# Optimization experiments

Measured on AMD Instinct MI355X. Metric: run time of the kernel, lower is better.

## Reference

```python
import jax, jax.numpy as jnp
import numpy as np

N_NODES = 100000
N_EDGES = 1600000
N_GRAPHS = 64
D_IN, D_HID, D_LAT = 2, 64, 32


def setup_inputs() -> dict:
    key = jax.random.key(0)
    k1, k2, k3, k4, k5, k6, k7 = jax.random.split(key, 7)
    x = jax.random.normal(k1, (N_NODES, D_IN), dtype=jnp.float32)
    edge_index = jax.random.randint(k2, (2, N_EDGES), 0, N_NODES, dtype=jnp.int64)
    batch = jnp.sort(jax.random.randint(k3, (N_NODES,), 0, N_GRAPHS, dtype=jnp.int64))
    # GCNConv params (glorot-ish scale)
    W1 = jax.random.normal(k4, (D_IN, D_HID), dtype=jnp.float32) * (1.0 / np.sqrt(D_IN))
    b1 = jnp.zeros((D_HID,), dtype=jnp.float32)
    W2 = jax.random.normal(k5, (D_HID, D_LAT), dtype=jnp.float32) * (1.0 / np.sqrt(D_HID))
    b2 = jnp.zeros((D_LAT,), dtype=jnp.float32)
    return {"x": x, "W1": W1, "b1": b1, "W2": W2, "b2": b2,
            "edge_index": edge_index, "batch": batch}


def _gcn_conv(x, W, b, src, dst, n_nodes):
    """PyG GCNConv: add self-loops, symmetric deg^-1/2 normalization, linear, scatter-add."""
    h = x @ W  # [N, d_out]
    loop = jnp.arange(n_nodes, dtype=src.dtype)
    src_f = jnp.concatenate([src, loop])
    dst_f = jnp.concatenate([dst, loop])
    deg = jax.ops.segment_sum(jnp.ones_like(dst_f, dtype=h.dtype), dst_f,
                              num_segments=n_nodes)  # in-degree incl. self-loop
    dis = jnp.where(deg > 0, jax.lax.rsqrt(deg), 0.0)
    norm = dis[src_f] * dis[dst_f]  # [E+N]
    msg = h[src_f] * norm[:, None]  # edge gather (memory-bound)
    out = jax.ops.segment_sum(msg, dst_f, num_segments=n_nodes)
    return out + b


def reference(x, W1, b1, W2, b2, edge_index, batch):
    src, dst = edge_index[0], edge_index[1]
    n = x.shape[0]
    h = jax.nn.relu(_gcn_conv(x, W1, b1, src, dst, n))
    z = _gcn_conv(h, W2, b2, src, dst, n)
    # global_mean_pool over graph ids
    sums = jax.ops.segment_sum(z, batch, num_segments=N_GRAPHS)
    cnts = jax.ops.segment_sum(jnp.ones((n,), dtype=z.dtype), batch,
                               num_segments=N_GRAPHS)
    return sums / jnp.maximum(cnts, 1.0)[:, None]
```

## Files before the change

kernel.cpp:

```cpp
#include <hip/hip_runtime.h>
#include <hip/hip_fp16.h>

#define N_NODES  100000
#define N_EDGES  1600000
#define N_GRAPHS 64
#define NBUCK    391
#define NBLK     256
#define CHUNK    (N_EDGES / NBLK)

#define OFF_GSTART 0
#define OFF_ROWPTR 128
#define OFF_DIS    100224
#define OFF_S      200320
#define OFF_CSR    400384
#define OFF_Q      2000384
#define OFF_BHIST  2000384
#define OFF_BOFFL  2100736
#define OFF_BSUM   2201088
#define OFF_BSTART 2201600
#define OFF_TMP    2202112

__device__ __forceinline__ int excl_scan_256(int v, int* wsum) {
  int t = threadIdx.x, lane = t & 63, w = t >> 6;
  int x = v;
#pragma unroll
  for (int off = 1; off < 64; off <<= 1) {
    int y = __shfl_up(x, off, 64);
    if (lane >= off) x += y;
  }
  if (lane == 63) wsum[w] = x;
  __syncthreads();
  if (t == 0) {
    int r = 0;
#pragma unroll
    for (int i = 0; i < 4; ++i) { int tv = wsum[i]; wsum[i] = r; r += tv; }
  }
  __syncthreads();
  return x - v + wsum[w];
}

__device__ __forceinline__ int excl_scan_512(int v, int* wsum) {
  int t = threadIdx.x, lane = t & 63, w = t >> 6;
  int x = v;
#pragma unroll
  for (int off = 1; off < 64; off <<= 1) {
    int y = __shfl_up(x, off, 64);
    if (lane >= off) x += y;
  }
  if (lane == 63) wsum[w] = x;
  __syncthreads();
  if (t == 0) {
    int r = 0;
#pragma unroll
    for (int i = 0; i < 8; ++i) { int tv = wsum[i]; wsum[i] = r; r += tv; }
  }
  __syncthreads();
  return x - v + wsum[w];
}

__global__ void k_hist(const int* __restrict__ dst, int* __restrict__ bhist) {
  __shared__ int hist[NBUCK];
  int t = threadIdx.x, k = blockIdx.x;
  for (int b = t; b < NBUCK; b += 256) hist[b] = 0;
  __syncthreads();
  int e0 = k * CHUNK, e1 = e0 + CHUNK;
  for (int e = e0 + t; e < e1; e += 256) atomicAdd(&hist[dst[e] >> 8], 1);
  __syncthreads();
  for (int b = t; b < NBUCK; b += 256) bhist[b * NBLK + k] = hist[b];
}

__global__ void k_bounds(const int* __restrict__ batch, int* __restrict__ gstart) {
  int i = blockIdx.x * 256 + threadIdx.x;
  if (i >= N_NODES) return;
  int bi = batch[i];
  if (i == 0) {
    for (int g = 0; g <= bi; ++g) gstart[g] = 0;
  } else {
    int bp = batch[i - 1];
    for (int g = bp + 1; g <= bi; ++g) gstart[g] = i;
  }
  if (i == N_NODES - 1) {
    for (int g = bi + 1; g <= N_GRAPHS; ++g) gstart[g] = N_NODES;
  }
}

__global__ void k_scan_a(const int* __restrict__ bhist, int* __restrict__ boffl,
                         int* __restrict__ bsum) {
  __shared__ int wsum[4];
  int t = threadIdx.x, b = blockIdx.x;
  int v = bhist[b * NBLK + t];
  int ex = excl_scan_256(v, wsum);
  boffl[b * NBLK + t] = ex;
  if (t == NBLK - 1) bsum[b] = ex + v;
}

__global__ void k_scan_b(const int* __restrict__ bsum, int* __restrict__ bstart) {
  __shared__ int wsum[8];
  int t = threadIdx.x;
  int v = (t < NBUCK) ? bsum[t] : 0;
  int ex = excl_scan_512(v, wsum);
  if (t <= NBUCK) bstart[t] = ex;
}

__global__ void k_scatter(const int* __restrict__ src, const int* __restrict__ dst,
                          const int* __restrict__ bstart, const int* __restrict__ boffl,
                          int* __restrict__ tmp) {
  __shared__ int sbase[NBUCK];
  __shared__ int fill[NBUCK];
  int t = threadIdx.x, k = blockIdx.x;
  for (int b = t; b < NBUCK; b += 256) {
    sbase[b] = bstart[b] + boffl[b * NBLK + k];
    fill[b] = 0;
  }
  __syncthreads();
  int e0 = k * CHUNK, e1 = e0 + CHUNK;
  for (int e = e0 + t; e < e1; e += 256) {
    int s_ = src[e], d_ = dst[e];
    int b = d_ >> 8;
    int pos = sbase[b] + atomicAdd(&fill[b], 1);
    tmp[pos] = (s_ << 8) | (d_ & 255);
  }
}

__global__ void k_fine(const int* __restrict__ tmp, const int* __restrict__ bstart,
                       const float* __restrict__ x, int* __restrict__ csr_src,
                       int* __restrict__ row_ptr, float* __restrict__ dis,
                       float2* __restrict__ s) {
  __shared__ int hist[256];
  __shared__ int fill[256];
  __shared__ int wsum[4];
  int t = threadIdx.x, b = blockIdx.x;
  int base_n = b << 8;
  int e0 = bstart[b], e1 = bstart[b + 1];
  hist[t] = 0;
  __syncthreads();
  for (int e = e0 + t; e < e1; e += 256) atomicAdd(&hist[tmp[e] & 255], 1);
  __syncthreads();
  int h = hist[t];
  int ex = excl_scan_256(h, wsum);
  hist[t] = ex;
  fill[t] = 0;
  int nn = min(256, N_NODES - base_n);
  if (t < nn) {
    int v = base_n + t;
    row_ptr[v] = e0 + ex;
    float dv = rsqrtf((float)(h + 1));
    dis[v] = dv;
    float2 xv = ((const float2*)x)[v];
    s[v] = make_float2(xv.x * dv, xv.y * dv);
  }
  if (b == NBUCK - 1 && t == 0) row_ptr[N_NODES] = e1;
  __syncthreads();
  for (int e = e0 + t; e < e1; e += 256) {
    int p = tmp[e];
    int fine = p & 255;
    int pos = e0 + hist[fine] + atomicAdd(&fill[fine], 1);
    csr_src[pos] = p >> 8;
  }
}

__global__ void k_layer1(const float2* __restrict__ s, const float* __restrict__ dis,
                         const int* __restrict__ row_ptr, const int* __restrict__ csr_src,
                         const float* __restrict__ W1, const float* __restrict__ b1,
                         const float* __restrict__ W2, __half2* __restrict__ qh) {
  __shared__ float sW1[128];
  __shared__ float sb1[64];
  __shared__ float sW2[2048];
  int tid = threadIdx.x;
  for (int i = tid; i < 128; i += 256) sW1[i] = W1[i];
  for (int i = tid; i < 64; i += 256) sb1[i] = b1[i];
  for (int i = tid; i < 2048; i += 256) sW2[i] = W2[i];
  __syncthreads();
  int v = blockIdx.x * 256 + tid;
  if (v >= N_NODES) return;
  int beg = row_ptr[v], end = row_ptr[v + 1];
  float2 sv = s[v];
  float t0 = sv.x, t1 = sv.y;
  int k = beg;
  for (; k + 4 <= end; k += 4) {
    int u0 = csr_src[k], u1 = csr_src[k + 1], u2 = csr_src[k + 2], u3 = csr_src[k + 3];
    float2 a = s[u0], b = s[u1], c = s[u2], d = s[u3];
    t0 += a.x + b.x + c.x + d.x;
    t1 += a.y + b.y + c.y + d.y;
  }
  for (; k < end; ++k) {
    float2 su = s[csr_src[k]];
    t0 += su.x;
    t1 += su.y;
  }
  float dv = dis[v];
  t0 *= dv;
  t1 *= dv;
  float acc[32];
#pragma unroll
  for (int m = 0; m < 32; ++m) acc[m] = 0.f;
  for (int j = 0; j < 64; ++j) {
    float r = fmaxf(fmaf(t0, sW1[j], fmaf(t1, sW1[64 + j], sb1[j])), 0.f);
#pragma unroll
    for (int m = 0; m < 32; ++m) acc[m] = fmaf(r, sW2[j * 32 + m], acc[m]);
  }
  int buf[16];
#pragma unroll
  for (int m = 0; m < 16; ++m) {
    __half2 h = __floats2half2_rn(acc[2 * m] * dv, acc[2 * m + 1] * dv);
    buf[m] = *reinterpret_cast<int*>(&h);
  }
  int4* dst4 = (int4*)&qh[v * 16];
  dst4[0] = make_int4(buf[0], buf[1], buf[2], buf[3]);
  dst4[1] = make_int4(buf[4], buf[5], buf[6], buf[7]);
  dst4[2] = make_int4(buf[8], buf[9], buf[10], buf[11]);
  dst4[3] = make_int4(buf[12], buf[13], buf[14], buf[15]);
}

__global__ void k_layer2(const __half2* __restrict__ qh, const float* __restrict__ dis,
                         const int* __restrict__ row_ptr, const int* __restrict__ csr_src,
                         const int* __restrict__ batch, float* __restrict__ pooled) {
  __shared__ float2 red[16][16];
  int t = threadIdx.x;
  int f2 = t & 15;
  int rg = t >> 4;
  int vb = blockIdx.x * 64;
  int nlast = min(vb + 63, N_NODES - 1);
  bool uniform = (batch[vb] == batch[nlast]);
  int v0 = vb + rg * 4;
  int v1 = min(v0 + 4, N_NODES);
  float2 acc = make_float2(0.f, 0.f);
  int curg = (v0 < N_NODES) ? batch[v0] : -1;
  for (int v = v0; v < v1; ++v) {
    if (!uniform) {
      int g = batch[v];
      if (g != curg) {
        atomicAdd(&pooled[curg * 32 + 2 * f2], acc.x);
        atomicAdd(&pooled[curg * 32 + 2 * f2 + 1], acc.y);
        acc = make_float2(0.f, 0.f);
        curg = g;
      }
    }
    int e0 = row_ptr[v], e1 = row_ptr[v + 1];
    float2 z = __half22float2(qh[v * 16 + f2]);
    int k = e0;
    for (; k + 4 <= e1; k += 4) {
      int u0 = csr_src[k], u1 = csr_src[k + 1], u2 = csr_src[k + 2], u3 = csr_src[k + 3];
      __half2 a = qh[u0 * 16 + f2];
      __half2 b = qh[u1 * 16 + f2];
      __half2 c = qh[u2 * 16 + f2];
      __half2 d = qh[u3 * 16 + f2];
      float2 fa = __half22float2(a), fb = __half22float2(b);
      float2 fc = __half22float2(c), fd = __half22float2(d);
      z.x += (fa.x + fb.x) + (fc.x + fd.x);
      z.y += (fa.y + fb.y) + (fc.y + fd.y);
    }
    for (; k < e1; ++k) {
      float2 f = __half22float2(qh[csr_src[k] * 16 + f2]);
      z.x += f.x;
      z.y += f.y;
    }
    float dv = dis[v];
    acc.x = fmaf(z.x, dv, acc.x);
    acc.y = fmaf(z.y, dv, acc.y);
  }
  if (uniform) {
    red[rg][f2] = acc;
    __syncthreads();
    if (t < 16) {
      float2 ssum = make_float2(0.f, 0.f);
#pragma unroll
      for (int r = 0; r < 16; ++r) {
        ssum.x += red[r][t].x;
        ssum.y += red[r][t].y;
      }
      int g = batch[vb];
      atomicAdd(&pooled[g * 32 + 2 * t], ssum.x);
      atomicAdd(&pooled[g * 32 + 2 * t + 1], ssum.y);
    }
  } else if (curg >= 0) {
    atomicAdd(&pooled[curg * 32 + 2 * f2], acc.x);
    atomicAdd(&pooled[curg * 32 + 2 * f2 + 1], acc.y);
  }
}

__global__ void k_final(float* __restrict__ out, const int* __restrict__ gstart,
                        const float* __restrict__ b2) {
  int i = blockIdx.x * 256 + threadIdx.x;
  if (i < N_GRAPHS * 32) {
    int g = i >> 5, l = i & 31;
    int c = gstart[g + 1] - gstart[g];
    out[i] = (c > 0) ? out[i] / (float)c + b2[l] : 0.f;
  }
}

extern "C" void kernel_launch(void* const* d_in, const int* in_sizes, int n_in,
                              void* d_out, int out_size, void* d_ws, size_t ws_size,
                              hipStream_t stream) {
  (void)in_sizes; (void)n_in; (void)out_size; (void)ws_size;
  const float* x   = (const float*)d_in[0];
  const float* W1  = (const float*)d_in[1];
  const float* b1  = (const float*)d_in[2];
  const float* W2  = (const float*)d_in[3];
  const float* b2  = (const float*)d_in[4];
  const int* edge  = (const int*)d_in[5];
  const int* batch = (const int*)d_in[6];
  const int* src = edge;
  const int* dst = edge + N_EDGES;
  float* out = (float*)d_out;

  int* ws      = (int*)d_ws;
  int* gstart  = ws + OFF_GSTART;
  int* row_ptr = ws + OFF_ROWPTR;
  float* dis   = (float*)(ws + OFF_DIS);
  float2* s    = (float2*)(ws + OFF_S);
  int* csr_src = ws + OFF_CSR;
  __half2* qh  = (__half2*)(ws + OFF_Q);
  int* bhist   = ws + OFF_BHIST;
  int* boffl   = ws + OFF_BOFFL;
  int* bsum    = ws + OFF_BSUM;
  int* bstart  = ws + OFF_BSTART;
  int* tmp     = ws + OFF_TMP;

  hipMemsetAsync(out, 0, (size_t)(N_GRAPHS * 32) * sizeof(float), stream);

  k_hist<<<NBLK, 256, 0, stream>>>(dst, bhist);
  k_bounds<<<(N_NODES + 255) / 256, 256, 0, stream>>>(batch, gstart);
  k_scan_a<<<NBUCK, 256, 0, stream>>>(bhist, boffl, bsum);
  k_scan_b<<<1, 512, 0, stream>>>(bsum, bstart);
  k_scatter<<<NBLK, 256, 0, stream>>>(src, dst, bstart, boffl, tmp);
  k_fine<<<NBUCK, 256, 0, stream>>>(tmp, bstart, x, csr_src, row_ptr, dis, s);
  k_layer1<<<(N_NODES + 255) / 256, 256, 0, stream>>>(s, dis, row_ptr, csr_src,
                                                      W1, b1, W2, qh);
  k_layer2<<<(N_NODES + 63) / 64, 256, 0, stream>>>(qh, dis, row_ptr, csr_src,
                                                    batch, out);
  k_final<<<8, 256, 0, stream>>>(out, gstart, b2);
}
```

Baseline: 110.6 us.

## Split layer-2 features into lo/hi half tables and fold small launches into scans

The layer-1 output is written as two separate half-precision tables, one per 16-feature half. Layer-2 blocks each gather only one half, with blocks for the same node range interleaved across halves, so each gathered row is 32 bytes and each table's working set is smaller and more cache-friendly. The graph-bounds computation moves into the first scan kernel, and the output zeroing moves into the second scan kernel, which removes one launch and one memset. Layer 1 also loads its weights as float4 from shared memory, and layer 2 unrolls the edge gather by 8. The cost is twice as many layer-2 blocks, each re-reading row_ptr and csr_src, and extra atomics into the pooled output.

```diff
diff --git a/kernel.cpp b/kernel.cpp
--- a/kernel.cpp
+++ b/kernel.cpp
@@ -7,13 +7,15 @@
 #define NBUCK    391
 #define NBLK     256
 #define CHUNK    (N_EDGES / NBLK)
+#define NODEBLK  1563
 
 #define OFF_GSTART 0
 #define OFF_ROWPTR 128
 #define OFF_DIS    100224
 #define OFF_S      200320
 #define OFF_CSR    400384
-#define OFF_Q      2000384
+#define OFF_QLO    2000384
+#define OFF_QHI    2800512
 #define OFF_BHIST  2000384
 #define OFF_BOFFL  2100736
 #define OFF_BSUM   2201088
@@ -69,34 +71,35 @@
   for (int b = t; b < NBUCK; b += 256) bhist[b * NBLK + k] = hist[b];
 }
 
-__global__ void k_bounds(const int* __restrict__ batch, int* __restrict__ gstart) {
-  int i = blockIdx.x * 256 + threadIdx.x;
-  if (i >= N_NODES) return;
-  int bi = batch[i];
-  if (i == 0) {
-    for (int g = 0; g <= bi; ++g) gstart[g] = 0;
-  } else {
-    int bp = batch[i - 1];
-    for (int g = bp + 1; g <= bi; ++g) gstart[g] = i;
-  }
-  if (i == N_NODES - 1) {
-    for (int g = bi + 1; g <= N_GRAPHS; ++g) gstart[g] = N_NODES;
-  }
-}
-
 __global__ void k_scan_a(const int* __restrict__ bhist, int* __restrict__ boffl,
-                         int* __restrict__ bsum) {
+                         int* __restrict__ bsum, const int* __restrict__ batch,
+                         int* __restrict__ gstart) {
   __shared__ int wsum[4];
   int t = threadIdx.x, b = blockIdx.x;
+  int i = b * 256 + t;
+  if (i < N_NODES) {
+    int bi = batch[i];
+    if (i == 0) {
+      for (int g = 0; g <= bi; ++g) gstart[g] = 0;
+    } else {
+      int bp = batch[i - 1];
+      for (int g = bp + 1; g <= bi; ++g) gstart[g] = i;
+    }
+    if (i == N_NODES - 1) {
+      for (int g = bi + 1; g <= N_GRAPHS; ++g) gstart[g] = N_NODES;
+    }
+  }
   int v = bhist[b * NBLK + t];
   int ex = excl_scan_256(v, wsum);
   boffl[b * NBLK + t] = ex;
   if (t == NBLK - 1) bsum[b] = ex + v;
 }
 
-__global__ void k_scan_b(const int* __restrict__ bsum, int* __restrict__ bstart) {
+__global__ void k_scan_b(const int* __restrict__ bsum, int* __restrict__ bstart,
+                         float* __restrict__ pooled) {
   __shared__ int wsum[8];
   int t = threadIdx.x;
+  for (int i = t; i < N_GRAPHS * 32; i += 512) pooled[i] = 0.f;
   int v = (t < NBUCK) ? bsum[t] : 0;
   int ex = excl_scan_512(v, wsum);
   if (t <= NBUCK) bstart[t] = ex;
@@ -162,14 +165,13 @@
 __global__ void k_layer1(const float2* __restrict__ s, const float* __restrict__ dis,
                          const int* __restrict__ row_ptr, const int* __restrict__ csr_src,
                          const float* __restrict__ W1, const float* __restrict__ b1,
-                         const float* __restrict__ W2, __half2* __restrict__ qh) {
-  __shared__ float sW1[128];
-  __shared__ float sb1[64];
-  __shared__ float sW2[2048];
+                         const float* __restrict__ W2, int4* __restrict__ q_lo,
+                         int4* __restrict__ q_hi) {
+  __shared__ float4 sWB[64];
+  __shared__ float4 sW2[512];
   int tid = threadIdx.x;
-  for (int i = tid; i < 128; i += 256) sW1[i] = W1[i];
-  for (int i = tid; i < 64; i += 256) sb1[i] = b1[i];
-  for (int i = tid; i < 2048; i += 256) sW2[i] = W2[i];
+  if (tid < 64) sWB[tid] = make_float4(W1[tid], W1[64 + tid], b1[tid], 0.f);
+  for (int i = tid; i < 512; i += 256) sW2[i] = ((const float4*)W2)[i];
   __syncthreads();
   int v = blockIdx.x * 256 + tid;
   if (v >= N_NODES) return;
@@ -180,8 +182,8 @@
   for (; k + 4 <= end; k += 4) {
     int u0 = csr_src[k], u1 = csr_src[k + 1], u2 = csr_src[k + 2], u3 = csr_src[k + 3];
     float2 a = s[u0], b = s[u1], c = s[u2], d = s[u3];
-    t0 += a.x + b.x + c.x + d.x;
-    t1 += a.y + b.y + c.y + d.y;
+    t0 += (a.x + b.x) + (c.x + d.x);
+    t1 += (a.y + b.y) + (c.y + d.y);
   }
   for (; k < end; ++k) {
     float2 su = s[csr_src[k]];
@@ -191,67 +193,94 @@
   float dv = dis[v];
   t0 *= dv;
   t1 *= dv;
-  float acc[32];
-#pragma unroll
-  for (int m = 0; m < 32; ++m) acc[m] = 0.f;
+  float4 a4[8];
+#pragma unroll
+  for (int m = 0; m < 8; ++m) a4[m] = make_float4(0.f, 0.f, 0.f, 0.f);
   for (int j = 0; j < 64; ++j) {
-    float r = fmaxf(fmaf(t0, sW1[j], fmaf(t1, sW1[64 + j], sb1[j])), 0.f);
-#pragma unroll
-    for (int m = 0; m < 32; ++m) acc[m] = fmaf(r, sW2[j * 32 + m], acc[m]);
-  }
-  int buf[16];
-#pragma unroll
-  for (int m = 0; m < 16; ++m) {
-    __half2 h = __floats2half2_rn(acc[2 * m] * dv, acc[2 * m + 1] * dv);
-    buf[m] = *reinterpret_cast<int*>(&h);
-  }
-  int4* dst4 = (int4*)&qh[v * 16];
-  dst4[0] = make_int4(buf[0], buf[1], buf[2], buf[3]);
-  dst4[1] = make_int4(buf[4], buf[5], buf[6], buf[7]);
-  dst4[2] = make_int4(buf[8], buf[9], buf[10], buf[11]);
-  dst4[3] = make_int4(buf[12], buf[13], buf[14], buf[15]);
-}
-
-__global__ void k_layer2(const __half2* __restrict__ qh, const float* __restrict__ dis,
-                         const int* __restrict__ row_ptr, const int* __restrict__ csr_src,
-                         const int* __restrict__ batch, float* __restrict__ pooled) {
-  __shared__ float2 red[16][16];
+    float4 wb = sWB[j];
+    float r = fmaxf(fmaf(t0, wb.x, fmaf(t1, wb.y, wb.z)), 0.f);
+#pragma unroll
+    for (int m = 0; m < 8; ++m) {
+      float4 w = sW2[j * 8 + m];
+      a4[m].x = fmaf(r, w.x, a4[m].x);
+      a4[m].y = fmaf(r, w.y, a4[m].y);
+      a4[m].z = fmaf(r, w.z, a4[m].z);
+      a4[m].w = fmaf(r, w.w, a4[m].w);
+    }
+  }
+  int pk[16];
+#pragma unroll
+  for (int m = 0; m < 8; ++m) {
+    __half2 h0 = __floats2half2_rn(a4[m].x * dv, a4[m].y * dv);
+    __half2 h1 = __floats2half2_rn(a4[m].z * dv, a4[m].w * dv);
+    pk[2 * m]     = *reinterpret_cast<int*>(&h0);
+    pk[2 * m + 1] = *reinterpret_cast<int*>(&h1);
+  }
+  q_lo[v * 2]     = make_int4(pk[0], pk[1], pk[2], pk[3]);
+  q_lo[v * 2 + 1] = make_int4(pk[4], pk[5], pk[6], pk[7]);
+  q_hi[v * 2]     = make_int4(pk[8], pk[9], pk[10], pk[11]);
+  q_hi[v * 2 + 1] = make_int4(pk[12], pk[13], pk[14], pk[15]);
+}
+
+__global__ void k_layer2(const __half2* __restrict__ q_lo, const __half2* __restrict__ q_hi,
+                         const float* __restrict__ dis, const int* __restrict__ row_ptr,
+                         const int* __restrict__ csr_src, const int* __restrict__ batch,
+                         float* __restrict__ pooled) {
+  __shared__ float2 red[32][8];
+  int w = blockIdx.x;
+  int h = (w & 7) >> 2;
+  int sub = (w >> 3) * 4 + (w & 3);
+  if (sub >= NODEBLK) return;
+  const __half2* q = h ? q_hi : q_lo;
   int t = threadIdx.x;
-  int f2 = t & 15;
-  int rg = t >> 4;
-  int vb = blockIdx.x * 64;
+  int fp = t & 7;
+  int rg = t >> 3;
+  int vb = sub * 64;
   int nlast = min(vb + 63, N_NODES - 1);
   bool uniform = (batch[vb] == batch[nlast]);
-  int v0 = vb + rg * 4;
-  int v1 = min(v0 + 4, N_NODES);
+  int v0 = vb + rg * 2;
+  int v1 = min(v0 + 2, N_NODES);
   float2 acc = make_float2(0.f, 0.f);
   int curg = (v0 < N_NODES) ? batch[v0] : -1;
+  int obase = h * 16 + 2 * fp;
   for (int v = v0; v < v1; ++v) {
     if (!uniform) {
       int g = batch[v];
       if (g != curg) {
-        atomicAdd(&pooled[curg * 32 + 2 * f2], acc.x);
-        atomicAdd(&pooled[curg * 32 + 2 * f2 + 1], acc.y);
+        atomicAdd(&pooled[curg * 32 + obase], acc.x);
+        atomicAdd(&pooled[curg * 32 + obase + 1], acc.y);
         acc = make_float2(0.f, 0.f);
         curg = g;
       }
     }
     int e0 = row_ptr[v], e1 = row_ptr[v + 1];
-    float2 z = __half22float2(qh[v * 16 + f2]);
+    float2 z = __half22float2(q[v * 8 + fp]);
     int k = e0;
+    for (; k + 8 <= e1; k += 8) {
+      int u0 = csr_src[k],     u1 = csr_src[k + 1], u2 = csr_src[k + 2], u3 = csr_src[k + 3];
+      int u4 = csr_src[k + 4], u5 = csr_src[k + 5], u6 = csr_src[k + 6], u7 = csr_src[k + 7];
+      float2 f0 = __half22float2(q[u0 * 8 + fp]);
+      float2 f1 = __half22float2(q[u1 * 8 + fp]);
+      float2 f2 = __half22float2(q[u2 * 8 + fp]);
+      float2 f3 = __half22float2(q[u3 * 8 + fp]);
+      float2 f4 = __half22float2(q[u4 * 8 + fp]);
+      float2 f5 = __half22float2(q[u5 * 8 + fp]);
+      float2 f6 = __half22float2(q[u6 * 8 + fp]);
+      float2 f7 = __half22float2(q[u7 * 8 + fp]);
+      z.x += ((f0.x + f1.x) + (f2.x + f3.x)) + ((f4.x + f5.x) + (f6.x + f7.x));
+      z.y += ((f0.y + f1.y) + (f2.y + f3.y)) + ((f4.y + f5.y) + (f6.y + f7.y));
+    }
     for (; k + 4 <= e1; k += 4) {
       int u0 = csr_src[k], u1 = csr_src[k + 1], u2 = csr_src[k + 2], u3 = csr_src[k + 3];
-      __half2 a = qh[u0 * 16 + f2];
-      __half2 b = qh[u1 * 16 + f2];
-      __half2 c = qh[u2 * 16 + f2];
-      __half2 d = qh[u3 * 16 + f2];
-      float2 fa = __half22float2(a), fb = __half22float2(b);
-      float2 fc = __half22float2(c), fd = __half22float2(d);
-      z.x += (fa.x + fb.x) + (fc.x + fd.x);
-      z.y += (fa.y + fb.y) + (fc.y + fd.y);
+      float2 f0 = __half22float2(q[u0 * 8 + fp]);
+      float2 f1 = __half22float2(q[u1 * 8 + fp]);
+      float2 f2 = __half22float2(q[u2 * 8 + fp]);
+      float2 f3 = __half22float2(q[u3 * 8 + fp]);
+      z.x += (f0.x + f1.x) + (f2.x + f3.x);
+      z.y += (f0.y + f1.y) + (f2.y + f3.y);
     }
     for (; k < e1; ++k) {
-      float2 f = __half22float2(qh[csr_src[k] * 16 + f2]);
+      float2 f = __half22float2(q[csr_src[k] * 8 + fp]);
       z.x += f.x;
       z.y += f.y;
     }
@@ -260,22 +289,22 @@
     acc.y = fmaf(z.y, dv, acc.y);
   }
   if (uniform) {
-    red[rg][f2] = acc;
+    red[rg][fp] = acc;
     __syncthreads();
-    if (t < 16) {
+    if (t < 8) {
       float2 ssum = make_float2(0.f, 0.f);
 #pragma unroll
-      for (int r = 0; r < 16; ++r) {
+      for (int r = 0; r < 32; ++r) {
         ssum.x += red[r][t].x;
         ssum.y += red[r][t].y;
       }
       int g = batch[vb];
-      atomicAdd(&pooled[g * 32 + 2 * t], ssum.x);
-      atomicAdd(&pooled[g * 32 + 2 * t + 1], ssum.y);
+      atomicAdd(&pooled[g * 32 + h * 16 + 2 * t], ssum.x);
+      atomicAdd(&pooled[g * 32 + h * 16 + 2 * t + 1], ssum.y);
     }
   } else if (curg >= 0) {
-    atomicAdd(&pooled[curg * 32 + 2 * f2], acc.x);
-    atomicAdd(&pooled[curg * 32 + 2 * f2 + 1], acc.y);
+    atomicAdd(&pooled[curg * 32 + obase], acc.x);
+    atomicAdd(&pooled[curg * 32 + obase + 1], acc.y);
   }
 }
 
@@ -310,24 +339,23 @@
   float* dis   = (float*)(ws + OFF_DIS);
   float2* s    = (float2*)(ws + OFF_S);
   int* csr_src = ws + OFF_CSR;
-  __half2* qh  = (__half2*)(ws + OFF_Q);
+  int4* q_lo4  = (int4*)(ws + OFF_QLO);
+  int4* q_hi4  = (int4*)(ws + OFF_QHI);
   int* bhist   = ws + OFF_BHIST;
   int* boffl   = ws + OFF_BOFFL;
   int* bsum    = ws + OFF_BSUM;
   int* bstart  = ws + OFF_BSTART;
   int* tmp     = ws + OFF_TMP;
 
-  hipMemsetAsync(out, 0, (size_t)(N_GRAPHS * 32) * sizeof(float), stream);
-
   k_hist<<<NBLK, 256, 0, stream>>>(dst, bhist);
-  k_bounds<<<(N_NODES + 255) / 256, 256, 0, stream>>>(batch, gstart);
-  k_scan_a<<<NBUCK, 256, 0, stream>>>(bhist, boffl, bsum);
-  k_scan_b<<<1, 512, 0, stream>>>(bsum, bstart);
+  k_scan_a<<<NBUCK, 256, 0, stream>>>(bhist, boffl, bsum, batch, gstart);
+  k_scan_b<<<1, 512, 0, stream>>>(bsum, bstart, out);
   k_scatter<<<NBLK, 256, 0, stream>>>(src, dst, bstart, boffl, tmp);
   k_fine<<<NBUCK, 256, 0, stream>>>(tmp, bstart, x, csr_src, row_ptr, dis, s);
   k_layer1<<<(N_NODES + 255) / 256, 256, 0, stream>>>(s, dis, row_ptr, csr_src,
-                                                      W1, b1, W2, qh);
-  k_layer2<<<(N_NODES + 63) / 64, 256, 0, stream>>>(qh, dis, row_ptr, csr_src,
-                                                    batch, out);
+                                                      W1, b1, W2, q_lo4, q_hi4);
+  const int n_wg2 = ((NODEBLK + 3) / 4) * 8;
+  k_layer2<<<n_wg2, 256, 0, stream>>>((const __half2*)q_lo4, (const __half2*)q_hi4,
+                                      dis, row_ptr, csr_src, batch, out);
   k_final<<<8, 256, 0, stream>>>(out, gstart, b2);
 }
```

Result: faster. 105.4 us (-4.8%).
